# Performance work log

Measured on AMD Instinct MI355X. Metric: run time of the kernel, lower is better.

Reference implementation:

```python
import jax, jax.numpy as jnp
import numpy as np

N_NODES = 100000
N_EDGES = 1600000
N_FEAT = 128
N_CLASSES = 10
N_GRAPHS = 256


def setup_inputs() -> dict:
    key = jax.random.key(0)
    ks = jax.random.split(key, 16)
    x = jax.random.normal(ks[0], (N_NODES, N_FEAT), dtype=jnp.float32)
    edge_index = jax.random.randint(ks[1], (2, N_EDGES), 0, N_NODES, dtype=jnp.int64)
    batch = jnp.sort(jax.random.randint(ks[2], (N_NODES,), 0, N_GRAPHS, dtype=jnp.int64))
    s = 0.1
    # GAT1: in=128 -> heads=8, out_per_head=8, concat -> 64
    W1 = jax.random.normal(ks[3], (N_FEAT, 64), dtype=jnp.float32) * s
    a_src1 = jax.random.normal(ks[4], (8, 8), dtype=jnp.float32) * s
    a_dst1 = jax.random.normal(ks[5], (8, 8), dtype=jnp.float32) * s
    b1 = jnp.zeros((64,), jnp.float32)
    # GAT2: in=64 -> heads=1, out=128
    W2 = jax.random.normal(ks[6], (64, 128), dtype=jnp.float32) * s
    a_src2 = jax.random.normal(ks[7], (1, 128), dtype=jnp.float32) * s
    a_dst2 = jax.random.normal(ks[8], (1, 128), dtype=jnp.float32) * s
    b2 = jnp.zeros((128,), jnp.float32)
    fc_w = jax.random.normal(ks[9], (128, N_CLASSES), dtype=jnp.float32) * s
    fc_b = jnp.zeros((N_CLASSES,), jnp.float32)
    return {"x": x, "edge_index": edge_index, "batch": batch,
            "W1": W1, "a_src1": a_src1, "a_dst1": a_dst1, "b1": b1,
            "W2": W2, "a_src2": a_src2, "a_dst2": a_dst2, "b2": b2,
            "fc_w": fc_w, "fc_b": fc_b}


def _segment_softmax(e, seg, n):
    # e: [E, H]; softmax over edges sharing the same destination node
    m = jax.ops.segment_max(e, seg, num_segments=n)
    m = jnp.where(jnp.isfinite(m), m, jnp.zeros_like(m))  # guard isolated nodes
    ex = jnp.exp(e - m[seg])
    s = jax.ops.segment_sum(ex, seg, num_segments=n)
    return ex / (s[seg] + jnp.asarray(1e-16, e.dtype))


def _gat_conv(x, src, dst, W, a_src, a_dst, bias):
    # PyG GATConv (eval mode, self-loops already appended to src/dst)
    H, C = a_src.shape
    n = x.shape[0]
    h = (x @ W).reshape(n, H, C)                      # [N,H,C]
    al_s = jnp.einsum('nhc,hc->nh', h, a_src)          # [N,H]
    al_d = jnp.einsum('nhc,hc->nh', h, a_dst)
    e = jax.nn.leaky_relu(al_s[src] + al_d[dst], 0.2)  # [E,H]
    alpha = _segment_softmax(e, dst, n)                # [E,H]
    out = jax.ops.segment_sum(h[src] * alpha[..., None], dst, num_segments=n)  # [N,H,C]
    return out.reshape(n, H * C) + bias                # concat=True (H=1 layer2 is identity reshape)


def reference(x, edge_index, batch, W1, a_src1, a_dst1, b1, W2, a_src2, a_dst2, b2, fc_w, fc_b):
    n = x.shape[0]
    loop = jnp.arange(n, dtype=edge_index.dtype)
    src = jnp.concatenate([edge_index[0], loop])       # add self-loops (PyG default)
    dst = jnp.concatenate([edge_index[1], loop])
    x1 = jax.nn.relu(_gat_conv(x, src, dst, W1, a_src1, a_dst1, b1))
    # dropout p=0.6 is identity in eval mode
    x2 = _gat_conv(x1, src, dst, W2, a_src2, a_dst2, b2)
    cnt = jax.ops.segment_sum(jnp.ones((n,), x2.dtype), batch, num_segments=N_GRAPHS)
    pooled = jax.ops.segment_sum(x2, batch, num_segments=N_GRAPHS) / jnp.maximum(cnt, 1.0)[:, None]
    logits = pooled @ fc_w + fc_b
    return jax.nn.log_softmax(logits, axis=1)
```

## Files before the change

kernel.cpp:

```cpp
#include <hip/hip_runtime.h>
#include <math.h>

typedef unsigned int uint;
typedef unsigned short ushort;
typedef unsigned char uchar;
typedef __attribute__((ext_vector_type(2))) float v2f;
typedef __attribute__((ext_vector_type(4))) _Float16 h4v;
typedef __attribute__((ext_vector_type(8))) _Float16 h8v;

#define S1 4.0f
#define S2 16.0f

template <bool HI>
__device__ inline v2f fp8x2f(uint u) {
    return __builtin_amdgcn_cvt_pk_f32_fp8((int)u, HI);
}

__global__ __launch_bounds__(256) void k_gemm1(const float* __restrict__ x,
                                               const float* __restrict__ W1,
                                               const float* __restrict__ as1,
                                               const float* __restrict__ ad1,
                                               uchar* __restrict__ rec1, int N) {
    __shared__ float sB[128 * 64];
    __shared__ float sA[64 * 68];
    const int t = threadIdx.x;
    const int n0 = blockIdx.x * 64;
    {
        const float4* w4 = (const float4*)W1;
        float4* s4 = (float4*)sB;
#pragma unroll
        for (int i = 0; i < 8; ++i) s4[t + i * 256] = w4[t + i * 256];
    }
    const int r0 = (t >> 3) * 2;
    const int c0 = (t & 7) * 8;
    float acc0[8] = {0, 0, 0, 0, 0, 0, 0, 0};
    float acc1[8] = {0, 0, 0, 0, 0, 0, 0, 0};
    for (int kb = 0; kb < 2; ++kb) {
        __syncthreads();
#pragma unroll
        for (int i = 0; i < 4; ++i) {
            int idx = t + i * 256;
            int r = idx >> 4, kc = idx & 15;
            int n = n0 + r;
            float4 v = make_float4(0.f, 0.f, 0.f, 0.f);
            if (n < N) v = ((const float4*)x)[(size_t)n * 32 + kb * 16 + kc];
            *(float4*)&sA[r * 68 + kc * 4] = v;
        }
        __syncthreads();
        const float* bptr = &sB[kb * 64 * 64];
#pragma unroll 8
        for (int kk = 0; kk < 64; ++kk) {
            float a0 = sA[r0 * 68 + kk];
            float a1 = sA[(r0 + 1) * 68 + kk];
            const float* bp = &bptr[kk * 64 + c0];
            float4 b0 = *(const float4*)bp;
            float4 b1v = *(const float4*)(bp + 4);
            acc0[0] += a0 * b0.x; acc0[1] += a0 * b0.y; acc0[2] += a0 * b0.z; acc0[3] += a0 * b0.w;
            acc0[4] += a0 * b1v.x; acc0[5] += a0 * b1v.y; acc0[6] += a0 * b1v.z; acc0[7] += a0 * b1v.w;
            acc1[0] += a1 * b0.x; acc1[1] += a1 * b0.y; acc1[2] += a1 * b0.z; acc1[3] += a1 * b0.w;
            acc1[4] += a1 * b1v.x; acc1[5] += a1 * b1v.y; acc1[6] += a1 * b1v.z; acc1[7] += a1 * b1v.w;
        }
    }
    float ps0 = 0.f, pd0 = 0.f, ps1 = 0.f, pd1 = 0.f;
#pragma unroll
    for (int i = 0; i < 8; ++i) {
        float ws = as1[c0 + i], wd = ad1[c0 + i];
        ps0 += acc0[i] * ws; pd0 += acc0[i] * wd;
        ps1 += acc1[i] * ws; pd1 += acc1[i] * wd;
    }
    int n = n0 + r0;
    int head = t & 7;
    if (n < N) {
        int q0 = 0, q1 = 0;
        q0 = __builtin_amdgcn_cvt_pk_fp8_f32(acc0[0] * S1, acc0[1] * S1, q0, false);
        q0 = __builtin_amdgcn_cvt_pk_fp8_f32(acc0[2] * S1, acc0[3] * S1, q0, true);
        q1 = __builtin_amdgcn_cvt_pk_fp8_f32(acc0[4] * S1, acc0[5] * S1, q1, false);
        q1 = __builtin_amdgcn_cvt_pk_fp8_f32(acc0[6] * S1, acc0[7] * S1, q1, true);
        uint2 p; p.x = (uint)q0; p.y = (uint)q1;
        uchar* rp = rec1 + (size_t)n * 128;
        *(uint2*)(rp + c0) = p;
        *(float*)(rp + 64 + head * 4) = ps0;
        *(float*)(rp + 96 + head * 4) = pd0;
    }
    if (n + 1 < N) {
        int q0 = 0, q1 = 0;
        q0 = __builtin_amdgcn_cvt_pk_fp8_f32(acc1[0] * S1, acc1[1] * S1, q0, false);
        q0 = __builtin_amdgcn_cvt_pk_fp8_f32(acc1[2] * S1, acc1[3] * S1, q0, true);
        q1 = __builtin_amdgcn_cvt_pk_fp8_f32(acc1[4] * S1, acc1[5] * S1, q1, false);
        q1 = __builtin_amdgcn_cvt_pk_fp8_f32(acc1[6] * S1, acc1[7] * S1, q1, true);
        uint2 p; p.x = (uint)q0; p.y = (uint)q1;
        uchar* rp = rec1 + (size_t)(n + 1) * 128;
        *(uint2*)(rp + c0) = p;
        *(float*)(rp + 64 + head * 4) = ps1;
        *(float*)(rp + 96 + head * 4) = pd1;
    }
}

__global__ __launch_bounds__(256) void k_gemm2(const _Float16* __restrict__ x1pre,
                                               const float* __restrict__ W2,
                                               const float* __restrict__ b1,
                                               const float* __restrict__ as2,
                                               const float* __restrict__ ad2,
                                               uchar* __restrict__ h2f8,
                                               float* __restrict__ al2s,
                                               float* __restrict__ al2d, int N) {
    __shared__ float sB[64 * 128];
    __shared__ float sA[64 * 68];
    const int t = threadIdx.x;
    const int n0 = blockIdx.x * 64;
    {
        const float4* w4 = (const float4*)W2;
        float4* s4 = (float4*)sB;
#pragma unroll
        for (int i = 0; i < 8; ++i) s4[t + i * 256] = w4[t + i * 256];
    }
#pragma unroll
    for (int i = 0; i < 4; ++i) {
        int idx = t + i * 256;
        int r = idx >> 4, kc = idx & 15;
        int n = n0 + r;
        float4 v = make_float4(0.f, 0.f, 0.f, 0.f);
        if (n < N) {
            h4v hv = *(const h4v*)(x1pre + (size_t)n * 64 + kc * 4);
            float4 bb = ((const float4*)b1)[kc];
            v.x = fmaxf((float)hv[0] + bb.x, 0.f);
            v.y = fmaxf((float)hv[1] + bb.y, 0.f);
            v.z = fmaxf((float)hv[2] + bb.z, 0.f);
            v.w = fmaxf((float)hv[3] + bb.w, 0.f);
        }
        *(float4*)&sA[r * 68 + kc * 4] = v;
    }
    __syncthreads();
    const int r0 = (t >> 3) * 2;
    const int cb = (t & 7) * 4;
    float acc0[16], acc1[16];
#pragma unroll
    for (int i = 0; i < 16; ++i) { acc0[i] = 0.f; acc1[i] = 0.f; }
#pragma unroll 4
    for (int k = 0; k < 64; ++k) {
        float a0 = sA[r0 * 68 + k];
        float a1 = sA[(r0 + 1) * 68 + k];
#pragma unroll
        for (int j = 0; j < 4; ++j) {
            float4 b = *(const float4*)&sB[k * 128 + cb + 32 * j];
            acc0[j * 4 + 0] += a0 * b.x; acc0[j * 4 + 1] += a0 * b.y;
            acc0[j * 4 + 2] += a0 * b.z; acc0[j * 4 + 3] += a0 * b.w;
            acc1[j * 4 + 0] += a1 * b.x; acc1[j * 4 + 1] += a1 * b.y;
            acc1[j * 4 + 2] += a1 * b.z; acc1[j * 4 + 3] += a1 * b.w;
        }
    }
    float ps0 = 0.f, pd0 = 0.f, ps1 = 0.f, pd1 = 0.f;
#pragma unroll
    for (int j = 0; j < 4; ++j)
#pragma unroll
        for (int i = 0; i < 4; ++i) {
            int cc = cb + 32 * j + i;
            float ws = as2[cc], wd = ad2[cc];
            ps0 += acc0[j * 4 + i] * ws; pd0 += acc0[j * 4 + i] * wd;
            ps1 += acc1[j * 4 + i] * ws; pd1 += acc1[j * 4 + i] * wd;
        }
#pragma unroll
    for (int off = 1; off < 8; off <<= 1) {
        ps0 += __shfl_xor(ps0, off); pd0 += __shfl_xor(pd0, off);
        ps1 += __shfl_xor(ps1, off); pd1 += __shfl_xor(pd1, off);
    }
    int n = n0 + r0;
    if (n < N) {
#pragma unroll
        for (int j = 0; j < 4; ++j) {
            int q = 0;
            q = __builtin_amdgcn_cvt_pk_fp8_f32(acc0[j * 4 + 0] * S2, acc0[j * 4 + 1] * S2, q, false);
            q = __builtin_amdgcn_cvt_pk_fp8_f32(acc0[j * 4 + 2] * S2, acc0[j * 4 + 3] * S2, q, true);
            *(uint*)&h2f8[(size_t)n * 128 + cb + 32 * j] = (uint)q;
        }
        if ((t & 7) == 0) { al2s[n] = ps0; al2d[n] = pd0; }
    }
    if (n + 1 < N) {
#pragma unroll
        for (int j = 0; j < 4; ++j) {
            int q = 0;
            q = __builtin_amdgcn_cvt_pk_fp8_f32(acc1[j * 4 + 0] * S2, acc1[j * 4 + 1] * S2, q, false);
            q = __builtin_amdgcn_cvt_pk_fp8_f32(acc1[j * 4 + 2] * S2, acc1[j * 4 + 3] * S2, q, true);
            *(uint*)&h2f8[(size_t)(n + 1) * 128 + cb + 32 * j] = (uint)q;
        }
        if ((t & 7) == 0) { al2s[n + 1] = ps1; al2d[n + 1] = pd1; }
    }
}


__global__ __launch_bounds__(256) void k_hist(const int* __restrict__ dst,
                                              int* __restrict__ counts,
                                              int E, int CH, int NB) {
    __shared__ int hist[784];
    int t = threadIdx.x, b = blockIdx.x;
    for (int k = t; k < NB; k += 256) hist[k] = 0;
    __syncthreads();
    int e0 = b * CH;
    int e1 = e0 + CH; if (e1 > E) e1 = E;
    for (int e = e0 + t; e < e1; e += 256)
        atomicAdd(&hist[dst[e] >> 7], 1);
    __syncthreads();
    for (int k = t; k < NB; k += 256) counts[(size_t)b * NB + k] = hist[k];
}

__global__ __launch_bounds__(256) void k_bscan(int* __restrict__ counts,
                                               int* __restrict__ btot,
                                               int C, int NB) {
    __shared__ int sh[256];
    int t = threadIdx.x, k = blockIdx.x;
    int v[4];
#pragma unroll
    for (int i = 0; i < 4; ++i) {
        int b = t * 4 + i;
        v[i] = (b < C) ? counts[(size_t)b * NB + k] : 0;
    }
    int s = v[0] + v[1] + v[2] + v[3];
    sh[t] = s;
    __syncthreads();
    int accv = s;
    for (int off = 1; off < 256; off <<= 1) {
        int u = (t >= off) ? sh[t - off] : 0;
        __syncthreads();
        accv += u;
        sh[t] = accv;
        __syncthreads();
    }
    int excl = accv - s;
#pragma unroll
    for (int i = 0; i < 4; ++i) {
        int b = t * 4 + i;
        if (b < C) counts[(size_t)b * NB + k] = excl;
        excl += v[i];
    }
    if (t == 255) btot[k] = accv;
}

__global__ __launch_bounds__(256) void k_bucket(const int* __restrict__ src,
                                                const int* __restrict__ dst,
                                                const int* __restrict__ counts,
                                                const int* __restrict__ btot,
                                                int* __restrict__ bbase,
                                                int* __restrict__ ebuf,
                                                int E, int CH, int NB) {
    __shared__ int pos[784];
    __shared__ int sh[256];
    __shared__ int bb[784];
    int t = threadIdx.x, b = blockIdx.x;
    int v[4];
#pragma unroll
    for (int i = 0; i < 4; ++i) {
        int k = t * 4 + i;
        v[i] = (k < NB) ? btot[k] : 0;
    }
    int s = v[0] + v[1] + v[2] + v[3];
    sh[t] = s;
    __syncthreads();
    int accv = s;
    for (int off = 1; off < 256; off <<= 1) {
        int u = (t >= off) ? sh[t - off] : 0;
        __syncthreads();
        accv += u;
        sh[t] = accv;
        __syncthreads();
    }
    int excl = accv - s;
#pragma unroll
    for (int i = 0; i < 4; ++i) {
        int k = t * 4 + i;
        if (k < NB) bb[k] = excl;
        excl += v[i];
    }
    __syncthreads();
    for (int k = t; k < NB; k += 256)
        pos[k] = bb[k] + counts[(size_t)b * NB + k];
    if (b == 0) {
        for (int k = t; k < NB; k += 256) bbase[k] = bb[k];
        if (t == 0) bbase[NB] = E;
    }
    __syncthreads();
    int e0 = b * CH;
    int e1 = e0 + CH; if (e1 > E) e1 = E;
    for (int e = e0 + t; e < e1; e += 256) {
        int d = dst[e], s2 = src[e];
        int p = atomicAdd(&pos[d >> 7], 1);
        ebuf[p] = (int)((uint)s2 | ((uint)(d & 127) << 25));
    }
}

__global__ __launch_bounds__(256) void k_csr(const int* __restrict__ bbase,
                                             const int* __restrict__ ebuf,
                                             int* __restrict__ row_ptr,
                                             int* __restrict__ col,
                                             int N, int E) {
    __shared__ int cnt[128];
    __shared__ int fill[128];
    __shared__ int rowb[128];
    __shared__ int sh[256];
    int t = threadIdx.x, k = blockIdx.x;
    int lo = bbase[k], hi = bbase[k + 1];
    int nlo = k << 7;
    int nn = N - nlo; if (nn > 128) nn = 128;
    if (t < 128) { cnt[t] = 0; fill[t] = 0; }
    __syncthreads();
    for (int i = lo + t; i < hi; i += 256)
        atomicAdd(&cnt[((uint)ebuf[i]) >> 25], 1);
    __syncthreads();
    int v = (t < nn) ? (cnt[t] + 1) : 0;
    sh[t] = v;
    __syncthreads();
    int accv = v;
    for (int off = 1; off < 256; off <<= 1) {
        int u = (t >= off) ? sh[t - off] : 0;
        __syncthreads();
        accv += u;
        sh[t] = accv;
        __syncthreads();
    }
    int fbase = lo + nlo;
    if (t < nn) {
        int rb = fbase + accv - v;
        rowb[t] = rb;
        row_ptr[nlo + t] = rb;
        col[rb + cnt[t]] = nlo + t;
    }
    if (k == 0 && t == 0) row_ptr[N] = E + N;
    __syncthreads();
    for (int i = lo + t; i < hi; i += 256) {
        uint e = (uint)ebuf[i];
        int j = (int)(e >> 25);
        int r = atomicAdd(&fill[j], 1);
        col[rowb[j] + r] = (int)(e & 0x1FFFFFFu);
    }
}

__global__ __launch_bounds__(256) void k_edge1(const uchar* __restrict__ rec1,
                                               const int* __restrict__ row_ptr,
                                               const int* __restrict__ col,
                                               _Float16* __restrict__ x1pre, int N) {
    int node = blockIdx.x * 4 + (threadIdx.x >> 6);
    if (node >= N) return;
    const int lane = threadIdx.x & 63;
    const int g = lane >> 4;
    const int k4 = lane & 15;
    const int hh = k4 >> 1;
    const uint co = (uint)(k4 * 4);
    const uint ao = 64u + (uint)(hh * 4);
    const float a_dh = *(const float*)(rec1 + (((size_t)node) << 7) + 96 + hh * 4);
    const int s0 = row_ptr[node], s1 = row_ptr[node + 1];
    float den_part = 0.f;
    v2f accL = {0.f, 0.f};
    v2f accH = {0.f, 0.f};
    for (int base = s0; base < s1; base += 64) {
        int cnt = s1 - base; if (cnt > 64) cnt = 64;
        int cntR = (cnt + 3) & ~3;
        int i = 0;
        for (; i + 16 <= cntR; i += 16) {
            int eA = base + i + g, eB = eA + 4, eC = eA + 8, eD = eA + 12;
            int xD = eD < s1 ? eD : s1 - 1;
            int cA = col[eA], cB = col[eB], cC = col[eC], cD = col[xD];
            const uchar* rA = rec1 + (((uint)cA) << 7);
            const uchar* rB = rec1 + (((uint)cB) << 7);
            const uchar* rC = rec1 + (((uint)cC) << 7);
            const uchar* rD = rec1 + (((uint)cD) << 7);
            uint hA = *(const uint*)(rA + co);
            uint hB = *(const uint*)(rB + co);
            uint hC = *(const uint*)(rC + co);
            uint hD = *(const uint*)(rD + co);
            float lA = *(const float*)(rA + ao) + a_dh;
            float lB = *(const float*)(rB + ao) + a_dh;
            float lC = *(const float*)(rC + ao) + a_dh;
            float lD = *(const float*)(rD + ao) + a_dh;
            lA = lA > 0.f ? lA : 0.2f * lA;
            lB = lB > 0.f ? lB : 0.2f * lB;
            lC = lC > 0.f ? lC : 0.2f * lC;
            lD = lD > 0.f ? lD : 0.2f * lD;
            float wA = __expf(lA);
            float wB = __expf(lB);
            float wC = __expf(lC);
            float wD = (eD < s1) ? __expf(lD) : 0.f;
            den_part += wA + wB + wC + wD;
            v2f wA2 = {wA, wA}, wB2 = {wB, wB}, wC2 = {wC, wC}, wD2 = {wD, wD};
            accL += wA2 * fp8x2f<false>(hA);
            accH += wA2 * fp8x2f<true>(hA);
            accL += wB2 * fp8x2f<false>(hB);
            accH += wB2 * fp8x2f<true>(hB);
            accL += wC2 * fp8x2f<false>(hC);
            accH += wC2 * fp8x2f<true>(hC);
            accL += wD2 * fp8x2f<false>(hD);
            accH += wD2 * fp8x2f<true>(hD);
        }
        int rem = cntR - i;
        if (rem & 8) {
            int eA = base + i + g, eB = eA + 4;
            int xB = eB < s1 ? eB : s1 - 1;
            int cA = col[eA], cB = col[xB];
            const uchar* rA = rec1 + (((uint)cA) << 7);
            const uchar* rB = rec1 + (((uint)cB) << 7);
            uint hA = *(const uint*)(rA + co);
            uint hB = *(const uint*)(rB + co);
            float lA = *(const float*)(rA + ao) + a_dh;
            float lB = *(const float*)(rB + ao) + a_dh;
            lA = lA > 0.f ? lA : 0.2f * lA;
            lB = lB > 0.f ? lB : 0.2f * lB;
            float wA = __expf(lA);
            float wB = (eB < s1) ? __expf(lB) : 0.f;
            den_part += wA + wB;
            v2f wA2 = {wA, wA}, wB2 = {wB, wB};
            accL += wA2 * fp8x2f<false>(hA);
            accH += wA2 * fp8x2f<true>(hA);
            accL += wB2 * fp8x2f<false>(hB);
            accH += wB2 * fp8x2f<true>(hB);
            i += 8;
        }
        if (rem & 4) {
            int eA = base + i + g;
            int xA = eA < s1 ? eA : s1 - 1;
            int cA = col[xA];
            const uchar* rA = rec1 + (((uint)cA) << 7);
            uint hA = *(const uint*)(rA + co);
            float lA = *(const float*)(rA + ao) + a_dh;
            lA = lA > 0.f ? lA : 0.2f * lA;
            float wA = (eA < s1) ? __expf(lA) : 0.f;
            den_part += wA;
            v2f wA2 = {wA, wA};
            accL += wA2 * fp8x2f<false>(hA);
            accH += wA2 * fp8x2f<true>(hA);
        }
    }
    float a0 = accL.x, a1 = accL.y, a2 = accH.x, a3 = accH.y;
    a0 += __shfl_xor(a0, 16); a0 += __shfl_xor(a0, 32);
    a1 += __shfl_xor(a1, 16); a1 += __shfl_xor(a1, 32);
    a2 += __shfl_xor(a2, 16); a2 += __shfl_xor(a2, 32);
    a3 += __shfl_xor(a3, 16); a3 += __shfl_xor(a3, 32);
    den_part += __shfl_xor(den_part, 16);
    den_part += __shfl_xor(den_part, 32);
    if (lane < 16) {
        float invd = 1.f / (den_part * S1);
        h4v o;
        o[0] = (_Float16)(a0 * invd);
        o[1] = (_Float16)(a1 * invd);
        o[2] = (_Float16)(a2 * invd);
        o[3] = (_Float16)(a3 * invd);
        *(h4v*)(x1pre + (size_t)node * 64 + co) = o;
    }
}

__global__ __launch_bounds__(256) void k_edge2(const uchar* __restrict__ h2f8,
                                               const float* __restrict__ al2s,
                                               const float* __restrict__ al2d,
                                               const int* __restrict__ row_ptr,
                                               const int* __restrict__ col,
                                               _Float16* __restrict__ x2, int N) {
    int node = blockIdx.x * 4 + (threadIdx.x >> 6);
    if (node >= N) return;
    const int lane = threadIdx.x & 63;
    const int g = lane >> 4;
    const int k8 = lane & 15;
    const uint co = (uint)(k8 * 8);
    const float a_d = al2d[node];
    const int s0 = row_ptr[node], s1 = row_ptr[node + 1];
    v2f acc0 = {0.f, 0.f}, acc1 = {0.f, 0.f}, acc2 = {0.f, 0.f}, acc3 = {0.f, 0.f};
    float den_part = 0.f;
    for (int base = s0; base < s1; base += 64) {
        int cnt = s1 - base; if (cnt > 64) cnt = 64;
        int cntR = (cnt + 3) & ~3;
        int i = 0;
        for (; i + 16 <= cntR; i += 16) {
            int eA = base + i + g, eB = eA + 4, eC = eA + 8, eD = eA + 12;
            int xD = eD < s1 ? eD : s1 - 1;
            int cA = col[eA], cB = col[eB], cC = col[eC], cD = col[xD];
            uint2 hA = *(const uint2*)(h2f8 + ((((uint)cA) << 7) | co));
            uint2 hB = *(const uint2*)(h2f8 + ((((uint)cB) << 7) | co));
            uint2 hC = *(const uint2*)(h2f8 + ((((uint)cC) << 7) | co));
            uint2 hD = *(const uint2*)(h2f8 + ((((uint)cD) << 7) | co));
            float lA = al2s[(uint)cA] + a_d;
            float lB = al2s[(uint)cB] + a_d;
            float lC = al2s[(uint)cC] + a_d;
            float lD = al2s[(uint)cD] + a_d;
            lA = lA > 0.f ? lA : 0.2f * lA;
            lB = lB > 0.f ? lB : 0.2f * lB;
            lC = lC > 0.f ? lC : 0.2f * lC;
            lD = lD > 0.f ? lD : 0.2f * lD;
            float wA = __expf(lA);
            float wB = __expf(lB);
            float wC = __expf(lC);
            float wD = (eD < s1) ? __expf(lD) : 0.f;
            den_part += wA + wB + wC + wD;
            v2f wA2 = {wA, wA}, wB2 = {wB, wB}, wC2 = {wC, wC}, wD2 = {wD, wD};
            acc0 += wA2 * fp8x2f<false>(hA.x);
            acc1 += wA2 * fp8x2f<true>(hA.x);
            acc2 += wA2 * fp8x2f<false>(hA.y);
            acc3 += wA2 * fp8x2f<true>(hA.y);
            acc0 += wB2 * fp8x2f<false>(hB.x);
            acc1 += wB2 * fp8x2f<true>(hB.x);
            acc2 += wB2 * fp8x2f<false>(hB.y);
            acc3 += wB2 * fp8x2f<true>(hB.y);
            acc0 += wC2 * fp8x2f<false>(hC.x);
            acc1 += wC2 * fp8x2f<true>(hC.x);
            acc2 += wC2 * fp8x2f<false>(hC.y);
            acc3 += wC2 * fp8x2f<true>(hC.y);
            acc0 += wD2 * fp8x2f<false>(hD.x);
            acc1 += wD2 * fp8x2f<true>(hD.x);
            acc2 += wD2 * fp8x2f<false>(hD.y);
            acc3 += wD2 * fp8x2f<true>(hD.y);
        }
        int rem = cntR - i;
        if (rem & 8) {
            int eA = base + i + g, eB = eA + 4;
            int xB = eB < s1 ? eB : s1 - 1;
            int cA = col[eA], cB = col[xB];
            uint2 hA = *(const uint2*)(h2f8 + ((((uint)cA) << 7) | co));
            uint2 hB = *(const uint2*)(h2f8 + ((((uint)cB) << 7) | co));
            float lA = al2s[(uint)cA] + a_d;
            float lB = al2s[(uint)cB] + a_d;
            lA = lA > 0.f ? lA : 0.2f * lA;
            lB = lB > 0.f ? lB : 0.2f * lB;
            float wA = __expf(lA);
            float wB = (eB < s1) ? __expf(lB) : 0.f;
            den_part += wA + wB;
            v2f wA2 = {wA, wA}, wB2 = {wB, wB};
            acc0 += wA2 * fp8x2f<false>(hA.x);
            acc1 += wA2 * fp8x2f<true>(hA.x);
            acc2 += wA2 * fp8x2f<false>(hA.y);
            acc3 += wA2 * fp8x2f<true>(hA.y);
            acc0 += wB2 * fp8x2f<false>(hB.x);
            acc1 += wB2 * fp8x2f<true>(hB.x);
            acc2 += wB2 * fp8x2f<false>(hB.y);
            acc3 += wB2 * fp8x2f<true>(hB.y);
            i += 8;
        }
        if (rem & 4) {
            int eA = base + i + g;
            int xA = eA < s1 ? eA : s1 - 1;
            int cA = col[xA];
            uint2 hA = *(const uint2*)(h2f8 + ((((uint)cA) << 7) | co));
            float lA = al2s[(uint)cA] + a_d;
            lA = lA > 0.f ? lA : 0.2f * lA;
            float wA = (eA < s1) ? __expf(lA) : 0.f;
            den_part += wA;
            v2f wA2 = {wA, wA};
            acc0 += wA2 * fp8x2f<false>(hA.x);
            acc1 += wA2 * fp8x2f<true>(hA.x);
            acc2 += wA2 * fp8x2f<false>(hA.y);
            acc3 += wA2 * fp8x2f<true>(hA.y);
        }
    }
    den_part += __shfl_xor(den_part, 16);
    den_part += __shfl_xor(den_part, 32);
    float r0 = acc0.x, r1 = acc0.y, r2 = acc1.x, r3 = acc1.y;
    float r4 = acc2.x, r5 = acc2.y, r6 = acc3.x, r7 = acc3.y;
    r0 += __shfl_xor(r0, 16); r0 += __shfl_xor(r0, 32);
    r1 += __shfl_xor(r1, 16); r1 += __shfl_xor(r1, 32);
    r2 += __shfl_xor(r2, 16); r2 += __shfl_xor(r2, 32);
    r3 += __shfl_xor(r3, 16); r3 += __shfl_xor(r3, 32);
    r4 += __shfl_xor(r4, 16); r4 += __shfl_xor(r4, 32);
    r5 += __shfl_xor(r5, 16); r5 += __shfl_xor(r5, 32);
    r6 += __shfl_xor(r6, 16); r6 += __shfl_xor(r6, 32);
    r7 += __shfl_xor(r7, 16); r7 += __shfl_xor(r7, 32);
    if (lane < 16) {
        float invd = 1.f / (den_part * S2);
        h8v o;
        o[0] = (_Float16)(r0 * invd);
        o[1] = (_Float16)(r1 * invd);
        o[2] = (_Float16)(r2 * invd);
        o[3] = (_Float16)(r3 * invd);
        o[4] = (_Float16)(r4 * invd);
        o[5] = (_Float16)(r5 * invd);
        o[6] = (_Float16)(r6 * invd);
        o[7] = (_Float16)(r7 * invd);
        *(h8v*)(x2 + (size_t)node * 128 + co) = o;
    }
}

__global__ __launch_bounds__(128) void k_pool(const _Float16* __restrict__ x2,
                                              const int* __restrict__ batch,
                                              float* __restrict__ pooled,
                                              float* __restrict__ cnt, int N) {
    int t = threadIdx.x;
    int nstart = blockIdx.x * 128;
    if (nstart >= N) return;
    int nend = nstart + 128;
    if (nend > N) nend = N;
    float acc = 0.f;
    int cur = batch[nstart];
    int count = 0;
    for (int n = nstart; n < nend; ++n) {
        int g = batch[n];
        if (g != cur) {
            atomicAdd(&pooled[(size_t)cur * 128 + t], acc);
            if (t == 0) atomicAdd(&cnt[cur], (float)count);
            acc = 0.f;
            count = 0;
            cur = g;
        }
        acc += (float)x2[(size_t)n * 128 + t];
        ++count;
    }
    atomicAdd(&pooled[(size_t)cur * 128 + t], acc);
    if (t == 0) atomicAdd(&cnt[cur], (float)count);
}

__global__ __launch_bounds__(64) void k_fc(const float* __restrict__ pooled,
                                           const float* __restrict__ cnt,
                                           const float* __restrict__ b2,
                                           const float* __restrict__ fcw,
                                           const float* __restrict__ fcb,
                                           float* __restrict__ out, int G) {
    int g = blockIdx.x;
    int c = threadIdx.x;
    float2 p = ((const float2*)pooled)[(size_t)g * 64 + c];
    float2 bb = ((const float2*)b2)[c];
    float inv = 1.f / fmaxf(cnt[g], 1.f);
    p.x = p.x * inv + bb.x;
    p.y = p.y * inv + bb.y;
    float l[10];
#pragma unroll
    for (int j = 0; j < 10; ++j)
        l[j] = p.x * fcw[(2 * c) * 10 + j] + p.y * fcw[(2 * c + 1) * 10 + j];
#pragma unroll
    for (int j = 0; j < 10; ++j)
        for (int off = 1; off < 64; off <<= 1) l[j] += __shfl_xor(l[j], off);
    if (c == 0) {
        float lj[10];
        float m = -1e30f;
#pragma unroll
        for (int j = 0; j < 10; ++j) {
            lj[j] = l[j] + fcb[j];
            m = fmaxf(m, lj[j]);
        }
        float s = 0.f;
#pragma unroll
        for (int j = 0; j < 10; ++j) s += expf(lj[j] - m);
        float ls = logf(s);
#pragma unroll
        for (int j = 0; j < 10; ++j) out[(size_t)g * 10 + j] = lj[j] - m - ls;
    }
}

extern "C" void kernel_launch(void* const* d_in, const int* in_sizes, int n_in,
                              void* d_out, int out_size, void* d_ws, size_t ws_size,
                              hipStream_t stream) {
    const float* x     = (const float*)d_in[0];
    const int*   ei    = (const int*)d_in[1];
    const int*   batch = (const int*)d_in[2];
    const float* W1    = (const float*)d_in[3];
    const float* as1   = (const float*)d_in[4];
    const float* ad1   = (const float*)d_in[5];
    const float* b1    = (const float*)d_in[6];
    const float* W2    = (const float*)d_in[7];
    const float* as2   = (const float*)d_in[8];
    const float* ad2   = (const float*)d_in[9];
    const float* b2    = (const float*)d_in[10];
    const float* fcw   = (const float*)d_in[11];
    const float* fcb   = (const float*)d_in[12];
    float* out = (float*)d_out;

    const int N = in_sizes[0] / 128;
    const int E = in_sizes[1] / 2;
    const int G = out_size / 10;
    const int* srcp = ei;
    const int* dstp = ei + E;

    float* wf = (float*)d_ws;
    uchar*    rec1  = (uchar*)wf;
    _Float16* x1pre = (_Float16*)(wf + (size_t)N * 32);
    _Float16* x2    = (_Float16*)wf;
    uchar*    h2f8  = (uchar*)(wf + (size_t)N * 128);
    float* al2s_  = wf + (size_t)N * 176;
    float* al2d_  = wf + (size_t)N * 177;
    float* pooled = wf + (size_t)N * 178;
    float* cnt    = pooled + (size_t)G * 128;

    const int NB = (N + 127) >> 7;
    const int C  = 1024;
    const int CH = (E + C - 1) / C;

    int* ib = (int*)(((uintptr_t)(cnt + G) + 15) & ~(uintptr_t)15);
    int* ebuf    = ib;
    int* counts  = ib + (size_t)E;
    int* btot    = counts + (size_t)C * NB;
    int* bbase   = btot + NB;
    int* row_ptr = bbase + NB + 1;
    int* col     = row_ptr + N + 1;

    size_t zbytes = ((size_t)G * 128 + G) * sizeof(float);
    (void)hipMemsetAsync(pooled, 0, zbytes, stream);

    const int nb64 = (N + 63) / 64;
    const int nb4  = (N + 3) / 4;
    const int nbP  = (N + 127) / 128;

    k_hist<<<C, 256, 0, stream>>>(dstp, counts, E, CH, NB);
    k_gemm1<<<nb64, 256, 0, stream>>>(x, W1, as1, ad1, rec1, N);
    k_bscan<<<NB, 256, 0, stream>>>(counts, btot, C, NB);
    k_bucket<<<C, 256, 0, stream>>>(srcp, dstp, counts, btot, bbase, ebuf, E, CH, NB);
    k_csr<<<NB, 256, 0, stream>>>(bbase, ebuf, row_ptr, col, N, E);
    k_edge1<<<nb4, 256, 0, stream>>>(rec1, row_ptr, col, x1pre, N);
    k_gemm2<<<nb64, 256, 0, stream>>>(x1pre, W2, b1, as2, ad2, h2f8, al2s_, al2d_, N);
    k_edge2<<<nb4, 256, 0, stream>>>(h2f8, al2s_, al2d_, row_ptr, col, x2, N);
    k_pool<<<nbP, 128, 0, stream>>>(x2, batch, pooled, cnt, N);
    k_fc<<<G, 64, 0, stream>>>(pooled, cnt, b2, fcw, fcb, out, G);
}
```

Baseline: 340.9 us.

## Fuse CSR build and pool+fc stages into cooperative kernels with grid syncs

Merges the histogram, bucket scan, bucketing and CSR construction kernels into one cooperative kernel that uses grid-wide syncs between phases. The bucket count drops from 1024 to 784 so every block can be co-resident. Pooling, the memset and the final FC/log-softmax are likewise fused into one cooperative kernel. The aim is to remove several kernel launch gaps and a memset. The cost is grid-sync overhead and reduced parallelism in the phases where only NB or G blocks do work.

New measurement: 758.2 us. 2.22x slower.

```diff
diff --git a/kernel.cpp b/kernel.cpp
--- a/kernel.cpp
+++ b/kernel.cpp
@@ -1,5 +1,8 @@
 #include <hip/hip_runtime.h>
+#include <hip/hip_cooperative_groups.h>
 #include <math.h>
+
+namespace cg = cooperative_groups;
 
 typedef unsigned int uint;
 typedef unsigned short ushort;
@@ -187,149 +190,137 @@
     }
 }
 
-
-__global__ __launch_bounds__(256) void k_hist(const int* __restrict__ dst,
-                                              int* __restrict__ counts,
-                                              int E, int CH, int NB) {
+__global__ __launch_bounds__(256) void k_graph(const int* __restrict__ src,
+                                               const int* __restrict__ dst,
+                                               int* __restrict__ counts,
+                                               int* __restrict__ btot,
+                                               int* __restrict__ ebuf,
+                                               int* __restrict__ row_ptr,
+                                               int* __restrict__ col,
+                                               int E, int CH, int NB, int N) {
     __shared__ int hist[784];
-    int t = threadIdx.x, b = blockIdx.x;
+    __shared__ int bb[784];
+    __shared__ int sh[256];
+    __shared__ int cnt[128];
+    __shared__ int fill[128];
+    __shared__ int rowb[128];
+    cg::grid_group grid = cg::this_grid();
+    const int t = threadIdx.x, b = blockIdx.x;
+    const int C = gridDim.x;
+    const int e0 = b * CH;
+    const int e1 = (e0 + CH < E) ? e0 + CH : E;
+
     for (int k = t; k < NB; k += 256) hist[k] = 0;
     __syncthreads();
-    int e0 = b * CH;
-    int e1 = e0 + CH; if (e1 > E) e1 = E;
     for (int e = e0 + t; e < e1; e += 256)
         atomicAdd(&hist[dst[e] >> 7], 1);
     __syncthreads();
     for (int k = t; k < NB; k += 256) counts[(size_t)b * NB + k] = hist[k];
-}
-
-__global__ __launch_bounds__(256) void k_bscan(int* __restrict__ counts,
-                                               int* __restrict__ btot,
-                                               int C, int NB) {
-    __shared__ int sh[256];
-    int t = threadIdx.x, k = blockIdx.x;
-    int v[4];
-#pragma unroll
-    for (int i = 0; i < 4; ++i) {
-        int b = t * 4 + i;
-        v[i] = (b < C) ? counts[(size_t)b * NB + k] : 0;
-    }
-    int s = v[0] + v[1] + v[2] + v[3];
-    sh[t] = s;
+    grid.sync();
+
+    if (b < NB) {
+        int v[4];
+#pragma unroll
+        for (int i = 0; i < 4; ++i) {
+            int kb = t * 4 + i;
+            v[i] = (kb < C) ? counts[(size_t)kb * NB + b] : 0;
+        }
+        int s = v[0] + v[1] + v[2] + v[3];
+        sh[t] = s;
+        __syncthreads();
+        int accv = s;
+        for (int off = 1; off < 256; off <<= 1) {
+            int u = (t >= off) ? sh[t - off] : 0;
+            __syncthreads();
+            accv += u;
+            sh[t] = accv;
+            __syncthreads();
+        }
+        int excl = accv - s;
+#pragma unroll
+        for (int i = 0; i < 4; ++i) {
+            int kb = t * 4 + i;
+            if (kb < C) counts[(size_t)kb * NB + b] = excl;
+            excl += v[i];
+        }
+        if (t == 255) btot[b] = accv;
+    }
+    grid.sync();
+
+    {
+        int v[4];
+#pragma unroll
+        for (int i = 0; i < 4; ++i) {
+            int k = t * 4 + i;
+            v[i] = (k < NB) ? btot[k] : 0;
+        }
+        int s = v[0] + v[1] + v[2] + v[3];
+        sh[t] = s;
+        __syncthreads();
+        int accv = s;
+        for (int off = 1; off < 256; off <<= 1) {
+            int u = (t >= off) ? sh[t - off] : 0;
+            __syncthreads();
+            accv += u;
+            sh[t] = accv;
+            __syncthreads();
+        }
+        int excl = accv - s;
+#pragma unroll
+        for (int i = 0; i < 4; ++i) {
+            int k = t * 4 + i;
+            if (k < NB) bb[k] = excl;
+            excl += v[i];
+        }
+    }
     __syncthreads();
-    int accv = s;
-    for (int off = 1; off < 256; off <<= 1) {
-        int u = (t >= off) ? sh[t - off] : 0;
-        __syncthreads();
-        accv += u;
-        sh[t] = accv;
-        __syncthreads();
-    }
-    int excl = accv - s;
-#pragma unroll
-    for (int i = 0; i < 4; ++i) {
-        int b = t * 4 + i;
-        if (b < C) counts[(size_t)b * NB + k] = excl;
-        excl += v[i];
-    }
-    if (t == 255) btot[k] = accv;
-}
-
-__global__ __launch_bounds__(256) void k_bucket(const int* __restrict__ src,
-                                                const int* __restrict__ dst,
-                                                const int* __restrict__ counts,
-                                                const int* __restrict__ btot,
-                                                int* __restrict__ bbase,
-                                                int* __restrict__ ebuf,
-                                                int E, int CH, int NB) {
-    __shared__ int pos[784];
-    __shared__ int sh[256];
-    __shared__ int bb[784];
-    int t = threadIdx.x, b = blockIdx.x;
-    int v[4];
-#pragma unroll
-    for (int i = 0; i < 4; ++i) {
-        int k = t * 4 + i;
-        v[i] = (k < NB) ? btot[k] : 0;
-    }
-    int s = v[0] + v[1] + v[2] + v[3];
-    sh[t] = s;
+
+    for (int k = t; k < NB; k += 256)
+        hist[k] = bb[k] + counts[(size_t)b * NB + k];
     __syncthreads();
-    int accv = s;
-    for (int off = 1; off < 256; off <<= 1) {
-        int u = (t >= off) ? sh[t - off] : 0;
-        __syncthreads();
-        accv += u;
-        sh[t] = accv;
-        __syncthreads();
-    }
-    int excl = accv - s;
-#pragma unroll
-    for (int i = 0; i < 4; ++i) {
-        int k = t * 4 + i;
-        if (k < NB) bb[k] = excl;
-        excl += v[i];
-    }
-    __syncthreads();
-    for (int k = t; k < NB; k += 256)
-        pos[k] = bb[k] + counts[(size_t)b * NB + k];
-    if (b == 0) {
-        for (int k = t; k < NB; k += 256) bbase[k] = bb[k];
-        if (t == 0) bbase[NB] = E;
-    }
-    __syncthreads();
-    int e0 = b * CH;
-    int e1 = e0 + CH; if (e1 > E) e1 = E;
     for (int e = e0 + t; e < e1; e += 256) {
         int d = dst[e], s2 = src[e];
-        int p = atomicAdd(&pos[d >> 7], 1);
+        int p = atomicAdd(&hist[d >> 7], 1);
         ebuf[p] = (int)((uint)s2 | ((uint)(d & 127) << 25));
     }
-}
-
-__global__ __launch_bounds__(256) void k_csr(const int* __restrict__ bbase,
-                                             const int* __restrict__ ebuf,
-                                             int* __restrict__ row_ptr,
-                                             int* __restrict__ col,
-                                             int N, int E) {
-    __shared__ int cnt[128];
-    __shared__ int fill[128];
-    __shared__ int rowb[128];
-    __shared__ int sh[256];
-    int t = threadIdx.x, k = blockIdx.x;
-    int lo = bbase[k], hi = bbase[k + 1];
-    int nlo = k << 7;
-    int nn = N - nlo; if (nn > 128) nn = 128;
-    if (t < 128) { cnt[t] = 0; fill[t] = 0; }
-    __syncthreads();
-    for (int i = lo + t; i < hi; i += 256)
-        atomicAdd(&cnt[((uint)ebuf[i]) >> 25], 1);
-    __syncthreads();
-    int v = (t < nn) ? (cnt[t] + 1) : 0;
-    sh[t] = v;
-    __syncthreads();
-    int accv = v;
-    for (int off = 1; off < 256; off <<= 1) {
-        int u = (t >= off) ? sh[t - off] : 0;
+    grid.sync();
+
+    if (b < NB) {
+        int lo = bb[b];
+        int hi = (b + 1 < NB) ? bb[b + 1] : E;
+        int nlo = b << 7;
+        int nn = N - nlo; if (nn > 128) nn = 128;
+        if (t < 128) { cnt[t] = 0; fill[t] = 0; }
         __syncthreads();
-        accv += u;
-        sh[t] = accv;
+        for (int i = lo + t; i < hi; i += 256)
+            atomicAdd(&cnt[((uint)ebuf[i]) >> 25], 1);
         __syncthreads();
-    }
-    int fbase = lo + nlo;
-    if (t < nn) {
-        int rb = fbase + accv - v;
-        rowb[t] = rb;
-        row_ptr[nlo + t] = rb;
-        col[rb + cnt[t]] = nlo + t;
-    }
-    if (k == 0 && t == 0) row_ptr[N] = E + N;
-    __syncthreads();
-    for (int i = lo + t; i < hi; i += 256) {
-        uint e = (uint)ebuf[i];
-        int j = (int)(e >> 25);
-        int r = atomicAdd(&fill[j], 1);
-        col[rowb[j] + r] = (int)(e & 0x1FFFFFFu);
+        int v = (t < nn) ? (cnt[t] + 1) : 0;
+        sh[t] = v;
+        __syncthreads();
+        int accv = v;
+        for (int off = 1; off < 256; off <<= 1) {
+            int u = (t >= off) ? sh[t - off] : 0;
+            __syncthreads();
+            accv += u;
+            sh[t] = accv;
+            __syncthreads();
+        }
+        int fbase = lo + nlo;
+        if (t < nn) {
+            int rb = fbase + accv - v;
+            rowb[t] = rb;
+            row_ptr[nlo + t] = rb;
+            col[rb + cnt[t]] = nlo + t;
+        }
+        if (b == 0 && t == 0) row_ptr[N] = E + N;
+        __syncthreads();
+        for (int i = lo + t; i < hi; i += 256) {
+            uint e = (uint)ebuf[i];
+            int j = (int)(e >> 25);
+            int r = atomicAdd(&fill[j], 1);
+            col[rowb[j] + r] = (int)(e & 0x1FFFFFFu);
+        }
     }
 }
 
@@ -572,68 +563,73 @@
     }
 }
 
-__global__ __launch_bounds__(128) void k_pool(const _Float16* __restrict__ x2,
-                                              const int* __restrict__ batch,
-                                              float* __restrict__ pooled,
-                                              float* __restrict__ cnt, int N) {
-    int t = threadIdx.x;
-    int nstart = blockIdx.x * 128;
-    if (nstart >= N) return;
-    int nend = nstart + 128;
-    if (nend > N) nend = N;
-    float acc = 0.f;
-    int cur = batch[nstart];
-    int count = 0;
-    for (int n = nstart; n < nend; ++n) {
-        int g = batch[n];
-        if (g != cur) {
-            atomicAdd(&pooled[(size_t)cur * 128 + t], acc);
-            if (t == 0) atomicAdd(&cnt[cur], (float)count);
-            acc = 0.f;
-            count = 0;
-            cur = g;
-        }
-        acc += (float)x2[(size_t)n * 128 + t];
-        ++count;
-    }
-    atomicAdd(&pooled[(size_t)cur * 128 + t], acc);
-    if (t == 0) atomicAdd(&cnt[cur], (float)count);
-}
-
-__global__ __launch_bounds__(64) void k_fc(const float* __restrict__ pooled,
-                                           const float* __restrict__ cnt,
-                                           const float* __restrict__ b2,
-                                           const float* __restrict__ fcw,
-                                           const float* __restrict__ fcb,
-                                           float* __restrict__ out, int G) {
-    int g = blockIdx.x;
-    int c = threadIdx.x;
-    float2 p = ((const float2*)pooled)[(size_t)g * 64 + c];
-    float2 bb = ((const float2*)b2)[c];
-    float inv = 1.f / fmaxf(cnt[g], 1.f);
-    p.x = p.x * inv + bb.x;
-    p.y = p.y * inv + bb.y;
-    float l[10];
-#pragma unroll
-    for (int j = 0; j < 10; ++j)
-        l[j] = p.x * fcw[(2 * c) * 10 + j] + p.y * fcw[(2 * c + 1) * 10 + j];
-#pragma unroll
-    for (int j = 0; j < 10; ++j)
-        for (int off = 1; off < 64; off <<= 1) l[j] += __shfl_xor(l[j], off);
-    if (c == 0) {
-        float lj[10];
-        float m = -1e30f;
-#pragma unroll
-        for (int j = 0; j < 10; ++j) {
-            lj[j] = l[j] + fcb[j];
-            m = fmaxf(m, lj[j]);
-        }
-        float s = 0.f;
-#pragma unroll
-        for (int j = 0; j < 10; ++j) s += expf(lj[j] - m);
-        float ls = logf(s);
-#pragma unroll
-        for (int j = 0; j < 10; ++j) out[(size_t)g * 10 + j] = lj[j] - m - ls;
+__global__ __launch_bounds__(128) void k_poolfc(const _Float16* __restrict__ x2,
+                                                const int* __restrict__ batch,
+                                                float* __restrict__ pooled,
+                                                float* __restrict__ cnt,
+                                                const float* __restrict__ b2,
+                                                const float* __restrict__ fcw,
+                                                const float* __restrict__ fcb,
+                                                float* __restrict__ out,
+                                                int N, int G) {
+    cg::grid_group grid = cg::this_grid();
+    const int t = threadIdx.x, b = blockIdx.x;
+    const int tot = G * 128 + G;
+    for (int i = b * 128 + t; i < tot; i += gridDim.x * 128) pooled[i] = 0.f;
+    grid.sync();
+    int nstart = b * 128;
+    if (nstart < N) {
+        int nend = nstart + 128;
+        if (nend > N) nend = N;
+        float acc = 0.f;
+        int cur = batch[nstart];
+        int count = 0;
+        for (int n = nstart; n < nend; ++n) {
+            int g = batch[n];
+            if (g != cur) {
+                atomicAdd(&pooled[(size_t)cur * 128 + t], acc);
+                if (t == 0) atomicAdd(&cnt[cur], (float)count);
+                acc = 0.f;
+                count = 0;
+                cur = g;
+            }
+            acc += (float)x2[(size_t)n * 128 + t];
+            ++count;
+        }
+        atomicAdd(&pooled[(size_t)cur * 128 + t], acc);
+        if (t == 0) atomicAdd(&cnt[cur], (float)count);
+    }
+    grid.sync();
+    if (b < G && t < 64) {
+        int g = b;
+        int c = t;
+        float2 p = ((const float2*)pooled)[(size_t)g * 64 + c];
+        float2 bb = ((const float2*)b2)[c];
+        float inv = 1.f / fmaxf(cnt[g], 1.f);
+        p.x = p.x * inv + bb.x;
+        p.y = p.y * inv + bb.y;
+        float l[10];
+#pragma unroll
+        for (int j = 0; j < 10; ++j)
+            l[j] = p.x * fcw[(2 * c) * 10 + j] + p.y * fcw[(2 * c + 1) * 10 + j];
+#pragma unroll
+        for (int j = 0; j < 10; ++j)
+            for (int off = 1; off < 64; off <<= 1) l[j] += __shfl_xor(l[j], off);
+        if (c == 0) {
+            float lj[10];
+            float m = -1e30f;
+#pragma unroll
+            for (int j = 0; j < 10; ++j) {
+                lj[j] = l[j] + fcb[j];
+                m = fmaxf(m, lj[j]);
+            }
+            float s = 0.f;
+#pragma unroll
+            for (int j = 0; j < 10; ++j) s += expf(lj[j] - m);
+            float ls = logf(s);
+#pragma unroll
+            for (int j = 0; j < 10; ++j) out[(size_t)g * 10 + j] = lj[j] - m - ls;
+        }
     }
 }
 
@@ -672,32 +668,41 @@
     float* cnt    = pooled + (size_t)G * 128;
 
     const int NB = (N + 127) >> 7;
-    const int C  = 1024;
-    const int CH = (E + C - 1) / C;
+    const int Cg = 784;
+    const int CHg = (E + Cg - 1) / Cg;
 
     int* ib = (int*)(((uintptr_t)(cnt + G) + 15) & ~(uintptr_t)15);
     int* ebuf    = ib;
     int* counts  = ib + (size_t)E;
-    int* btot    = counts + (size_t)C * NB;
-    int* bbase   = btot + NB;
-    int* row_ptr = bbase + NB + 1;
+    int* btot    = counts + (size_t)Cg * NB;
+    int* row_ptr = btot + NB;
     int* col     = row_ptr + N + 1;
-
-    size_t zbytes = ((size_t)G * 128 + G) * sizeof(float);
-    (void)hipMemsetAsync(pooled, 0, zbytes, stream);
 
     const int nb64 = (N + 63) / 64;
     const int nb4  = (N + 3) / 4;
     const int nbP  = (N + 127) / 128;
 
-    k_hist<<<C, 256, 0, stream>>>(dstp, counts, E, CH, NB);
     k_gemm1<<<nb64, 256, 0, stream>>>(x, W1, as1, ad1, rec1, N);
-    k_bscan<<<NB, 256, 0, stream>>>(counts, btot, C, NB);
-    k_bucket<<<C, 256, 0, stream>>>(srcp, dstp, counts, btot, bbase, ebuf, E, CH, NB);
-    k_csr<<<NB, 256, 0, stream>>>(bbase, ebuf, row_ptr, col, N, E);
+
+    {
+        int Ev = E, CHv = CHg, NBv = NB, Nv = N;
+        void* gargs[] = {(void*)&srcp, (void*)&dstp, (void*)&counts, (void*)&btot,
+                         (void*)&ebuf, (void*)&row_ptr, (void*)&col,
+                         (void*)&Ev, (void*)&CHv, (void*)&NBv, (void*)&Nv};
+        (void)hipLaunchCooperativeKernel((void*)k_graph, dim3(Cg), dim3(256),
+                                         gargs, 0, stream);
+    }
+
     k_edge1<<<nb4, 256, 0, stream>>>(rec1, row_ptr, col, x1pre, N);
     k_gemm2<<<nb64, 256, 0, stream>>>(x1pre, W2, b1, as2, ad2, h2f8, al2s_, al2d_, N);
     k_edge2<<<nb4, 256, 0, stream>>>(h2f8, al2s_, al2d_, row_ptr, col, x2, N);
-    k_pool<<<nbP, 128, 0, stream>>>(x2, batch, pooled, cnt, N);
-    k_fc<<<G, 64, 0, stream>>>(pooled, cnt, b2, fcw, fcb, out, G);
+
+    {
+        int Nv = N, Gv = G;
+        void* pargs[] = {(void*)&x2, (void*)&batch, (void*)&pooled, (void*)&cnt,
+                         (void*)&b2, (void*)&fcw, (void*)&fcb, (void*)&out,
+                         (void*)&Nv, (void*)&Gv};
+        (void)hipLaunchCooperativeKernel((void*)k_poolfc, dim3(nbP), dim3(128),
+                                         pargs, 0, stream);
+    }
 }
```

## Fuse histogram into gemm1 launch and merge pooling with FC per graph

Applied to the files above, without the earlier changes.

Runs the edge-destination histogram as extra blocks of the first GEMM kernel so both independent tasks share a single launch and can overlap. Replaces the atomic-based pooling kernel, its memset and the separate FC kernel with one kernel per graph that binary-searches the sorted batch array for its node range, sums the features directly and applies the FC and log-softmax. This removes two launches, a memset and global atomics. In exchange, pooling now uses only one block per graph, so each of the 256 blocks serially reads a few hundred rows, which may lower parallelism.

Result: no change. 343.9 us (+0.9%).

```diff
diff --git a/kernel.cpp b/kernel.cpp
--- a/kernel.cpp
+++ b/kernel.cpp
@@ -16,14 +16,30 @@
     return __builtin_amdgcn_cvt_pk_f32_fp8((int)u, HI);
 }
 
-__global__ __launch_bounds__(256) void k_gemm1(const float* __restrict__ x,
-                                               const float* __restrict__ W1,
-                                               const float* __restrict__ as1,
-                                               const float* __restrict__ ad1,
-                                               uchar* __restrict__ rec1, int N) {
+__global__ __launch_bounds__(256) void k_g1h(const float* __restrict__ x,
+                                             const float* __restrict__ W1,
+                                             const float* __restrict__ as1,
+                                             const float* __restrict__ ad1,
+                                             uchar* __restrict__ rec1,
+                                             const int* __restrict__ dst,
+                                             int* __restrict__ counts,
+                                             int N, int E, int CH, int NB, int GB) {
     __shared__ float sB[128 * 64];
     __shared__ float sA[64 * 68];
     const int t = threadIdx.x;
+    if (blockIdx.x >= GB) {
+        int b = blockIdx.x - GB;
+        int* hist = (int*)sB;
+        for (int k = t; k < NB; k += 256) hist[k] = 0;
+        __syncthreads();
+        int e0 = b * CH;
+        int e1 = e0 + CH; if (e1 > E) e1 = E;
+        for (int e = e0 + t; e < e1; e += 256)
+            atomicAdd(&hist[dst[e] >> 7], 1);
+        __syncthreads();
+        for (int k = t; k < NB; k += 256) counts[(size_t)b * NB + k] = hist[k];
+        return;
+    }
     const int n0 = blockIdx.x * 64;
     {
         const float4* w4 = (const float4*)W1;
@@ -187,21 +203,6 @@
     }
 }
 
-
-__global__ __launch_bounds__(256) void k_hist(const int* __restrict__ dst,
-                                              int* __restrict__ counts,
-                                              int E, int CH, int NB) {
-    __shared__ int hist[784];
-    int t = threadIdx.x, b = blockIdx.x;
-    for (int k = t; k < NB; k += 256) hist[k] = 0;
-    __syncthreads();
-    int e0 = b * CH;
-    int e1 = e0 + CH; if (e1 > E) e1 = E;
-    for (int e = e0 + t; e < e1; e += 256)
-        atomicAdd(&hist[dst[e] >> 7], 1);
-    __syncthreads();
-    for (int k = t; k < NB; k += 256) counts[(size_t)b * NB + k] = hist[k];
-}
 
 __global__ __launch_bounds__(256) void k_bscan(int* __restrict__ counts,
                                                int* __restrict__ btot,
@@ -572,68 +573,59 @@
     }
 }
 
-__global__ __launch_bounds__(128) void k_pool(const _Float16* __restrict__ x2,
-                                              const int* __restrict__ batch,
-                                              float* __restrict__ pooled,
-                                              float* __restrict__ cnt, int N) {
-    int t = threadIdx.x;
-    int nstart = blockIdx.x * 128;
-    if (nstart >= N) return;
-    int nend = nstart + 128;
-    if (nend > N) nend = N;
-    float acc = 0.f;
-    int cur = batch[nstart];
-    int count = 0;
-    for (int n = nstart; n < nend; ++n) {
-        int g = batch[n];
-        if (g != cur) {
-            atomicAdd(&pooled[(size_t)cur * 128 + t], acc);
-            if (t == 0) atomicAdd(&cnt[cur], (float)count);
-            acc = 0.f;
-            count = 0;
-            cur = g;
-        }
-        acc += (float)x2[(size_t)n * 128 + t];
-        ++count;
-    }
-    atomicAdd(&pooled[(size_t)cur * 128 + t], acc);
-    if (t == 0) atomicAdd(&cnt[cur], (float)count);
-}
-
-__global__ __launch_bounds__(64) void k_fc(const float* __restrict__ pooled,
-                                           const float* __restrict__ cnt,
-                                           const float* __restrict__ b2,
-                                           const float* __restrict__ fcw,
-                                           const float* __restrict__ fcb,
-                                           float* __restrict__ out, int G) {
-    int g = blockIdx.x;
-    int c = threadIdx.x;
-    float2 p = ((const float2*)pooled)[(size_t)g * 64 + c];
-    float2 bb = ((const float2*)b2)[c];
-    float inv = 1.f / fmaxf(cnt[g], 1.f);
-    p.x = p.x * inv + bb.x;
-    p.y = p.y * inv + bb.y;
-    float l[10];
-#pragma unroll
-    for (int j = 0; j < 10; ++j)
-        l[j] = p.x * fcw[(2 * c) * 10 + j] + p.y * fcw[(2 * c + 1) * 10 + j];
-#pragma unroll
-    for (int j = 0; j < 10; ++j)
-        for (int off = 1; off < 64; off <<= 1) l[j] += __shfl_xor(l[j], off);
-    if (c == 0) {
-        float lj[10];
-        float m = -1e30f;
-#pragma unroll
-        for (int j = 0; j < 10; ++j) {
-            lj[j] = l[j] + fcb[j];
-            m = fmaxf(m, lj[j]);
-        }
-        float s = 0.f;
-#pragma unroll
-        for (int j = 0; j < 10; ++j) s += expf(lj[j] - m);
-        float ls = logf(s);
-#pragma unroll
-        for (int j = 0; j < 10; ++j) out[(size_t)g * 10 + j] = lj[j] - m - ls;
+__global__ __launch_bounds__(128) void k_poolfc(const _Float16* __restrict__ x2,
+                                                const int* __restrict__ batch,
+                                                const float* __restrict__ b2,
+                                                const float* __restrict__ fcw,
+                                                const float* __restrict__ fcb,
+                                                float* __restrict__ out,
+                                                int N, int G) {
+    __shared__ float sp[128];
+    const int g = blockIdx.x;
+    const int t = threadIdx.x;
+    int lo = 0, hi = N;
+    while (lo < hi) { int m = (lo + hi) >> 1; if (batch[m] < g) lo = m + 1; else hi = m; }
+    const int s = lo;
+    hi = N;
+    while (lo < hi) { int m = (lo + hi) >> 1; if (batch[m] < g + 1) lo = m + 1; else hi = m; }
+    const int e = lo;
+    float a0 = 0.f, a1 = 0.f, a2 = 0.f, a3 = 0.f;
+    int n = s;
+    for (; n + 4 <= e; n += 4) {
+        a0 += (float)x2[(size_t)(n + 0) * 128 + t];
+        a1 += (float)x2[(size_t)(n + 1) * 128 + t];
+        a2 += (float)x2[(size_t)(n + 2) * 128 + t];
+        a3 += (float)x2[(size_t)(n + 3) * 128 + t];
+    }
+    for (; n < e; ++n) a0 += (float)x2[(size_t)n * 128 + t];
+    float inv = 1.f / fmaxf((float)(e - s), 1.f);
+    sp[t] = (a0 + a1 + a2 + a3) * inv + b2[t];
+    __syncthreads();
+    if (t < 64) {
+        int c = t;
+        float2 p = ((const float2*)sp)[c];
+        float l[10];
+#pragma unroll
+        for (int j = 0; j < 10; ++j)
+            l[j] = p.x * fcw[(2 * c) * 10 + j] + p.y * fcw[(2 * c + 1) * 10 + j];
+#pragma unroll
+        for (int j = 0; j < 10; ++j)
+            for (int off = 1; off < 64; off <<= 1) l[j] += __shfl_xor(l[j], off);
+        if (c == 0) {
+            float lj[10];
+            float m = -1e30f;
+#pragma unroll
+            for (int j = 0; j < 10; ++j) {
+                lj[j] = l[j] + fcb[j];
+                m = fmaxf(m, lj[j]);
+            }
+            float sde = 0.f;
+#pragma unroll
+            for (int j = 0; j < 10; ++j) sde += expf(lj[j] - m);
+            float ls = logf(sde);
+#pragma unroll
+            for (int j = 0; j < 10; ++j) out[(size_t)g * 10 + j] = lj[j] - m - ls;
+        }
     }
 }
 
@@ -668,14 +660,12 @@
     uchar*    h2f8  = (uchar*)(wf + (size_t)N * 128);
     float* al2s_  = wf + (size_t)N * 176;
     float* al2d_  = wf + (size_t)N * 177;
-    float* pooled = wf + (size_t)N * 178;
-    float* cnt    = pooled + (size_t)G * 128;
 
     const int NB = (N + 127) >> 7;
     const int C  = 1024;
     const int CH = (E + C - 1) / C;
 
-    int* ib = (int*)(((uintptr_t)(cnt + G) + 15) & ~(uintptr_t)15);
+    int* ib = (int*)(((uintptr_t)(wf + (size_t)N * 178) + 15) & ~(uintptr_t)15);
     int* ebuf    = ib;
     int* counts  = ib + (size_t)E;
     int* btot    = counts + (size_t)C * NB;
@@ -683,21 +673,16 @@
     int* row_ptr = bbase + NB + 1;
     int* col     = row_ptr + N + 1;
 
-    size_t zbytes = ((size_t)G * 128 + G) * sizeof(float);
-    (void)hipMemsetAsync(pooled, 0, zbytes, stream);
-
     const int nb64 = (N + 63) / 64;
     const int nb4  = (N + 3) / 4;
-    const int nbP  = (N + 127) / 128;
-
-    k_hist<<<C, 256, 0, stream>>>(dstp, counts, E, CH, NB);
-    k_gemm1<<<nb64, 256, 0, stream>>>(x, W1, as1, ad1, rec1, N);
+
+    k_g1h<<<nb64 + C, 256, 0, stream>>>(x, W1, as1, ad1, rec1, dstp, counts,
+                                        N, E, CH, NB, nb64);
     k_bscan<<<NB, 256, 0, stream>>>(counts, btot, C, NB);
     k_bucket<<<C, 256, 0, stream>>>(srcp, dstp, counts, btot, bbase, ebuf, E, CH, NB);
     k_csr<<<NB, 256, 0, stream>>>(bbase, ebuf, row_ptr, col, N, E);
     k_edge1<<<nb4, 256, 0, stream>>>(rec1, row_ptr, col, x1pre, N);
     k_gemm2<<<nb64, 256, 0, stream>>>(x1pre, W2, b1, as2, ad2, h2f8, al2s_, al2d_, N);
     k_edge2<<<nb4, 256, 0, stream>>>(h2f8, al2s_, al2d_, row_ptr, col, x2, N);
-    k_pool<<<nbP, 128, 0, stream>>>(x2, batch, pooled, cnt, N);
-    k_fc<<<G, 64, 0, stream>>>(pooled, cnt, b2, fcw, fcb, out, G);
-}
+    k_poolfc<<<G, 128, 0, stream>>>(x2, batch, b2, fcw, fcb, out, N, G);
+}
```
